# Performance work log

Hardware: AMD Instinct MI355X
Metric: run time of the kernel (lower is better)

Reference implementation:

```python
import jax, jax.numpy as jnp
import numpy as np

B, S, D, H, L, V = 8, 512, 1024, 16, 12, 30145
FF = 4 * D
NL = 2  # n_langs
EPS = 1e-12


def _ln(x, g, b):
    m = jnp.mean(x, axis=-1, keepdims=True)
    v = jnp.var(x, axis=-1, keepdims=True)
    return (x - m) * jax.lax.rsqrt(v + EPS) * g + b


def setup_inputs() -> dict:
    key = jax.random.key(0)
    ks = iter(jax.random.split(key, 32))
    std, estd = 0.02, 0.02
    d = {
        "input_ids": jax.random.randint(next(ks), (B, S), 0, V),
        "langs": jax.random.randint(next(ks), (B, S), 0, NL),
        "attention_mask": jnp.ones((B, S), jnp.float32),
        "word_emb": jax.random.normal(next(ks), (V, D), jnp.float32) * estd,
        "pos_emb": jax.random.normal(next(ks), (S, D), jnp.float32) * estd,
        "lang_emb": jax.random.normal(next(ks), (NL, D), jnp.float32) * estd,
        "ln_emb_g": jnp.ones((D,), jnp.float32),
        "ln_emb_b": jnp.zeros((D,), jnp.float32),
        "Wq": jax.random.normal(next(ks), (L, D, D), jnp.float32) * std,
        "bq": jnp.zeros((L, D), jnp.float32),
        "Wk": jax.random.normal(next(ks), (L, D, D), jnp.float32) * std,
        "bk": jnp.zeros((L, D), jnp.float32),
        "Wv": jax.random.normal(next(ks), (L, D, D), jnp.float32) * std,
        "bv": jnp.zeros((L, D), jnp.float32),
        "Wo": jax.random.normal(next(ks), (L, D, D), jnp.float32) * std,
        "bo": jnp.zeros((L, D), jnp.float32),
        "ln1_g": jnp.ones((L, D), jnp.float32),
        "ln1_b": jnp.zeros((L, D), jnp.float32),
        "W1": jax.random.normal(next(ks), (L, D, FF), jnp.float32) * std,
        "b1": jnp.zeros((L, FF), jnp.float32),
        "W2": jax.random.normal(next(ks), (L, FF, D), jnp.float32) * std,
        "b2": jnp.zeros((L, D), jnp.float32),
        "ln2_g": jnp.ones((L, D), jnp.float32),
        "ln2_b": jnp.zeros((L, D), jnp.float32),
    }
    return d


def reference(input_ids, langs, attention_mask, word_emb, pos_emb, lang_emb,
              ln_emb_g, ln_emb_b, Wq, bq, Wk, bk, Wv, bv, Wo, bo,
              ln1_g, ln1_b, W1, b1, W2, b2, ln2_g, ln2_b):
    dh = D // H
    scale = 1.0 / np.sqrt(dh).astype(np.float32)
    # embeddings: word + position + language, then LayerNorm, then pad-mask
    x = word_emb[input_ids] + pos_emb[None, :, :] + lang_emb[langs]  # [B,S,D]
    x = _ln(x, ln_emb_g, ln_emb_b)
    fmask = attention_mask  # [B,S], 1=keep
    x = x * fmask[:, :, None]
    neg = (-1e30) * (1.0 - fmask)[:, None, None, :]  # [B,1,1,S] additive mask

    def layer(x, p):
        Wq_, bq_, Wk_, bk_, Wv_, bv_, Wo_, bo_, g1, gb1, W1_, b1_, W2_, b2_, g2, gb2 = p
        q = ((x @ Wq_ + bq_) * scale).reshape(B, S, H, dh)
        k = (x @ Wk_ + bk_).reshape(B, S, H, dh)
        v = (x @ Wv_ + bv_).reshape(B, S, H, dh)
        scores = jnp.einsum('bqhd,bkhd->bhqk', q, k) + neg
        w = jax.nn.softmax(scores, axis=-1)
        ctx = jnp.einsum('bhqk,bkhd->bqhd', w, v).reshape(B, S, D)
        x = _ln(x + ctx @ Wo_ + bo_, g1, gb1)
        h = jax.nn.gelu(x @ W1_ + b1_, approximate=False)  # erf gelu as in source
        x = _ln(x + h @ W2_ + b2_, g2, gb2)
        x = x * fmask[:, :, None]
        return x, None

    params = (Wq, bq, Wk, bk, Wv, bv, Wo, bo, ln1_g, ln1_b, W1, b1, W2, b2, ln2_g, ln2_b)
    x, _ = jax.lax.scan(layer, x, params)
    return x
```

## Files before the change

### kernel.cpp

```cpp
#include <hip/hip_runtime.h>
#include <math.h>

typedef float  f32x4  __attribute__((ext_vector_type(4)));
typedef __bf16 bf16x8 __attribute__((ext_vector_type(8)));
typedef __bf16 bf16x4 __attribute__((ext_vector_type(4)));

#define DEV __device__ __forceinline__

DEV f32x4 mfma16(bf16x8 a, bf16x8 b, f32x4 c) {
    return __builtin_amdgcn_mfma_f32_16x16x32_bf16(a, b, c, 0, 0, 0);
}

DEV void async16(const void* g, void* l) {
    __builtin_amdgcn_global_load_lds((const __attribute__((address_space(1))) void*)g,
                                     (__attribute__((address_space(3))) void*)l, 16, 0, 0);
}

constexpr int B_  = 8;
constexpr int S_  = 512;
constexpr int D_  = 1024;
constexpr int H_  = 16;
constexpr int FF_ = 4096;
constexpr int ROWS = B_ * S_;

__global__ __launch_bounds__(256)
void embed_ln_kernel(const int* __restrict__ ids, const int* __restrict__ lgs,
                     const float* __restrict__ fmask,
                     const float* __restrict__ wemb, const float* __restrict__ pemb,
                     const float* __restrict__ lemb,
                     const float* __restrict__ g, const float* __restrict__ bb,
                     __bf16* __restrict__ xb)
{
    __shared__ float2 red[4];
    const int row = blockIdx.x;
    const int s   = row & (S_ - 1);
    const int t   = threadIdx.x;
    const int lane = t & 63, w = t >> 6;
    const int id = ids[row], lg = lgs[row];

    float4 wv = *(const float4*)(wemb + ((size_t)id << 10) + t * 4);
    float4 pv = *(const float4*)(pemb + ((size_t)s  << 10) + t * 4);
    float4 lv = *(const float4*)(lemb + ((size_t)lg << 10) + t * 4);
    float a[4] = { wv.x + pv.x + lv.x, wv.y + pv.y + lv.y,
                   wv.z + pv.z + lv.z, wv.w + pv.w + lv.w };

    float sm = a[0] + a[1] + a[2] + a[3];
    float sq = a[0]*a[0] + a[1]*a[1] + a[2]*a[2] + a[3]*a[3];
#pragma unroll
    for (int o = 32; o > 0; o >>= 1) { sm += __shfl_down(sm, o); sq += __shfl_down(sq, o); }
    if (lane == 0) red[w] = make_float2(sm, sq);
    __syncthreads();
    float ts = red[0].x + red[1].x + red[2].x + red[3].x;
    float tq = red[0].y + red[1].y + red[2].y + red[3].y;
    float mean = ts * (1.0f / D_);
    float var  = tq * (1.0f / D_) - mean * mean;
    float rs   = rsqrtf(var + 1e-12f);
    float fm   = fmask[row];

    float4 gv = *(const float4*)(g  + t * 4);
    float4 bv = *(const float4*)(bb + t * 4);
    bf16x4 ob;
    ob[0] = (__bf16)(((a[0]-mean)*rs*gv.x + bv.x) * fm);
    ob[1] = (__bf16)(((a[1]-mean)*rs*gv.y + bv.y) * fm);
    ob[2] = (__bf16)(((a[2]-mean)*rs*gv.z + bv.z) * fm);
    ob[3] = (__bf16)(((a[3]-mean)*rs*gv.w + bv.w) * fm);
    *(bf16x4*)(xb + ((size_t)row << 10) + t * 4) = ob;
}

template<int NP>
__global__ __launch_bounds__(128)
void ln_resN_kernel(const __bf16* __restrict__ xres, const __bf16* __restrict__ yp,
                    const float* __restrict__ g, const float* __restrict__ bb,
                    const float* __restrict__ fmask,
                    __bf16* __restrict__ xb_out, float* __restrict__ fout)
{
    constexpr size_t MN = (size_t)ROWS * D_;
    __shared__ float2 red[2];
    const int row = blockIdx.x;
    const int t   = threadIdx.x;
    const int lane = t & 63, w = t >> 6;
    const size_t base = ((size_t)row << 10) + t * 8;

    bf16x8 xv = *(const bf16x8*)(xres + base);
    float a[8];
#pragma unroll
    for (int j = 0; j < 8; ++j) a[j] = (float)xv[j];
#pragma unroll
    for (int pslice = 0; pslice < NP; ++pslice) {
        bf16x8 yv = *(const bf16x8*)(yp + base + (size_t)pslice * MN);
#pragma unroll
        for (int j = 0; j < 8; ++j) a[j] += (float)yv[j];
    }

    float sm = 0.f, sq = 0.f;
#pragma unroll
    for (int j = 0; j < 8; ++j) { sm += a[j]; sq += a[j] * a[j]; }
#pragma unroll
    for (int o = 32; o > 0; o >>= 1) { sm += __shfl_down(sm, o); sq += __shfl_down(sq, o); }
    if (lane == 0) red[w] = make_float2(sm, sq);
    __syncthreads();
    float ts = red[0].x + red[1].x;
    float tq = red[0].y + red[1].y;
    float mean = ts * (1.0f / D_);
    float var  = tq * (1.0f / D_) - mean * mean;
    float rs   = rsqrtf(var + 1e-12f);
    float fm   = fmask ? fmask[row] : 1.0f;

    float4 gv0 = *(const float4*)(g  + t * 8);
    float4 gv1 = *(const float4*)(g  + t * 8 + 4);
    float4 bv0 = *(const float4*)(bb + t * 8);
    float4 bv1 = *(const float4*)(bb + t * 8 + 4);
    float gg[8] = { gv0.x, gv0.y, gv0.z, gv0.w, gv1.x, gv1.y, gv1.z, gv1.w };
    float bbv[8] = { bv0.x, bv0.y, bv0.z, bv0.w, bv1.x, bv1.y, bv1.z, bv1.w };

    float o[8];
    bf16x8 ob;
#pragma unroll
    for (int j = 0; j < 8; ++j) {
        o[j] = ((a[j] - mean) * rs * gg[j] + bbv[j]) * fm;
        ob[j] = (__bf16)o[j];
    }
    *(bf16x8*)(xb_out + base) = ob;
    if (fout) {
        *(float4*)(fout + base)     = make_float4(o[0], o[1], o[2], o[3]);
        *(float4*)(fout + base + 4) = make_float4(o[4], o[5], o[6], o[7]);
    }
}

__global__ __launch_bounds__(256)
void conv_all_kernel(const float* __restrict__ Wq, const float* __restrict__ Wk,
                     const float* __restrict__ Wv, const float* __restrict__ Wo,
                     const float* __restrict__ W1, const float* __restrict__ W2,
                     __bf16* __restrict__ qkvT, __bf16* __restrict__ woT,
                     __bf16* __restrict__ w1T, __bf16* __restrict__ w2T)
{
    __shared__ unsigned int tile32[64 * 34];
    const int id = blockIdx.x;
    const int l  = id / 768;
    int t = id - l * 768;
    const size_t woff = (size_t)l * D_ * D_;
    const size_t foff = (size_t)l * D_ * FF_;
    const float* src; __bf16* dst; int K, N;
    if (t < 256) {
        const int m = t >> 6; t &= 63; K = 1024; N = 1024;
        src = ((m == 0) ? Wq : (m == 1) ? Wk : (m == 2) ? Wv : Wo) + woff;
        dst = (m == 3) ? (woT + woff)
                       : (qkvT + (size_t)l * 3 * D_ * D_ + (size_t)m * D_ * D_);
    } else if (t < 512) {
        t -= 256; K = 1024; N = 4096; src = W1 + foff; dst = w1T + foff;
    } else {
        t -= 512; K = 4096; N = 1024; src = W2 + foff; dst = w2T + foff;
    }
    const int ksup = K >> 8;
    const int tk = t % ksup, tn = t / ksup;
    const int k0s = tk << 8, n0t = tn << 6;
    const int tt = threadIdx.x;

    const int kp = tt >> 4;
    const int nq = tt & 15;
    const int swzw = (nq >> 2) << 2;
    const int nr = tt >> 3;
    const int kc = tt & 7;

    bf16x8 ob[2][4];
#pragma unroll
    for (int i4 = 0; i4 < 4; ++i4) {
        const int k0t = k0s + i4 * 64;
#pragma unroll
        for (int i = 0; i < 2; ++i) {
            const int k0 = i * 32 + kp * 2;
            const float4 r0 = *(const float4*)(src + (size_t)(k0t + k0)     * N + n0t + nq * 4);
            const float4 r1 = *(const float4*)(src + (size_t)(k0t + k0 + 1) * N + n0t + nq * 4);
            const int j = (i * 16 + kp) ^ swzw;
            const float lo[4] = { r0.x, r0.y, r0.z, r0.w };
            const float hi[4] = { r1.x, r1.y, r1.z, r1.w };
#pragma unroll
            for (int c = 0; c < 4; ++c) {
                const int n = nq * 4 + c;
                union { unsigned int u; __bf16 b[2]; } pk;
                pk.b[0] = (__bf16)lo[c];
                pk.b[1] = (__bf16)hi[c];
                tile32[n * 34 + j] = pk.u;
            }
        }
        __syncthreads();
#pragma unroll
        for (int pp = 0; pp < 2; ++pp) {
            const int n = pp * 32 + nr;
            const int jb = (kc * 4) ^ ((n >> 4) << 2);
            const unsigned int* tp = tile32 + n * 34 + jb;
            union { unsigned int u[4]; bf16x8 v; } o;
            o.u[0] = tp[0]; o.u[1] = tp[1]; o.u[2] = tp[2]; o.u[3] = tp[3];
            ob[pp][i4] = o.v;
        }
        __syncthreads();
    }
#pragma unroll
    for (int pp = 0; pp < 2; ++pp) {
        const int n = pp * 32 + nr;
        __bf16* drow = dst + (size_t)(n0t + n) * K + k0s + kc * 8;
#pragma unroll
        for (int i4 = 0; i4 < 4; ++i4)
            *(bf16x8*)(drow + i4 * 64) = ob[pp][i4];
    }
}

template<int EPI>
__global__ __launch_bounds__(512, 2)
void gemm256_kernel(const __bf16* __restrict__ A, const __bf16* __restrict__ Bt,
                    const float* __restrict__ b0, const float* __restrict__ b1,
                    const float* __restrict__ b2,
                    __bf16* __restrict__ o0, __bf16* __restrict__ o1,
                    __bf16* __restrict__ o2, __bf16* __restrict__ oP,
                    int M, int N, int K, int Kloc, int nTn, int tiles)
{
    __shared__ __bf16 lds[65536];
    const int tid  = threadIdx.x;
    const int lane = tid & 63;
    const int w    = tid >> 6;
    const int wr   = w >> 2, wc = w & 3;

    const int nwg = gridDim.x, bid = blockIdx.x;
    const int cpx = nwg >> 3;
    const int bswz = (bid & 7) * cpx + (bid >> 3);
    const int slice = bswz / tiles;
    const int tile  = bswz % tiles;
    const int bm = tile / nTn, bn = tile % nTn;
    const int m0 = bm << 8, n0 = bn << 8;
    const int ks = slice * Kloc;

    const int rrT = tid >> 3;
    const size_t swzK  = (size_t)(((tid & 7) ^ (rrT & 7)) * 8);
    const size_t aoff0 = (size_t)rrT * K + swzK;
    const size_t boff0 = (size_t)((rrT >> 5) * 64 + (rrT & 31)) * K + swzK;
    const size_t boff1 = (size_t)(((rrT >> 5) + 2) * 64 + (rrT & 31)) * K + swzK;
    const int wub = w * 512;

    const int aread = (wr * 64 + (lane & 15)) * 64;
    const int bread = (wc * 32 + (lane & 15)) * 64;
    const int csw0 = ((      (lane >> 4) * 16) ^ ((lane & 7) << 4)) >> 1;
    const int csw1 = ((64 +  (lane >> 4) * 16) ^ ((lane & 7) << 4)) >> 1;

    f32x4 acc[8][4] = {};
    bf16x8 a_[4][2], b_[2][2];

#define ST_A(p,h,kt) do {                                                     \
    const size_t gb = (size_t)(m0 + (h) * 64) * K + (kt);                     \
    async16(A + gb + aoff0,                  lds + ((p)*2+(h))*8192 + wub);   \
    async16(A + gb + (size_t)128*K + aoff0,  lds + ((p)*2+(h))*8192 + 4096 + wub); \
} while (0)
#define ST_B(p,h,kt) do {                                                     \
    const size_t gb = (size_t)(n0 + (h) * 32) * K + (kt);                     \
    async16(Bt + gb + boff0, lds + 32768 + ((p)*2+(h))*8192 + wub);           \
    async16(Bt + gb + boff1, lds + 32768 + ((p)*2+(h))*8192 + 4096 + wub);    \
} while (0)
#define DS_A(p,h) do {                                                        \
    const __bf16* base_ = lds + ((p)*2+(h))*8192 + aread;                     \
    _Pragma("unroll") for (int m_ = 0; m_ < 4; ++m_) {                        \
        a_[m_][0] = *(const bf16x8*)(base_ + m_*1024 + csw0);                 \
        a_[m_][1] = *(const bf16x8*)(base_ + m_*1024 + csw1);                 \
    }                                                                         \
} while (0)
#define DS_B(p,h) do {                                                        \
    const __bf16* base_ = lds + 32768 + ((p)*2+(h))*8192 + bread;             \
    _Pragma("unroll") for (int n_ = 0; n_ < 2; ++n_) {                        \
        b_[n_][0] = *(const bf16x8*)(base_ + n_*1024 + csw0);                 \
        b_[n_][1] = *(const bf16x8*)(base_ + n_*1024 + csw1);                 \
    }                                                                         \
} while (0)
#define MM(mb,nb) do {                                                        \
    _Pragma("unroll") for (int m_ = 0; m_ < 4; ++m_)                          \
    _Pragma("unroll") for (int n_ = 0; n_ < 2; ++n_)                          \
    _Pragma("unroll") for (int k_ = 0; k_ < 2; ++k_)                          \
        acc[(mb)+m_][(nb)+n_] = mfma16(a_[m_][k_], b_[n_][k_], acc[(mb)+m_][(nb)+n_]); \
} while (0)
#define SYNC do { __builtin_amdgcn_s_barrier();                               \
    asm volatile("s_waitcnt lgkmcnt(0)" ::: "memory");                        \
    __builtin_amdgcn_s_setprio(1); } while (0)
#define PEND do { __builtin_amdgcn_s_setprio(0);                              \
    __builtin_amdgcn_s_barrier(); } while (0)

    ST_A(0,0, ks);      ST_B(0,1, ks);      ST_A(0,1, ks);      ST_B(0,0, ks);
    ST_A(1,0, ks + 64); ST_B(1,1, ks + 64); ST_A(1,1, ks + 64);
    asm volatile("s_waitcnt vmcnt(6)" ::: "memory");
    __builtin_amdgcn_s_barrier();

    const int nIter = Kloc >> 7;
    for (int i = 0; i < nIter; ++i) {
        const bool nl = (i != nIter - 1);
        const int kt1 = ks + (2*i+1) * 64;
        const int kt2 = ks + (2*i+2) * 64;
        const int kt3 = kt2 + 64;
        DS_A(0,0); DS_B(0,0); ST_B(1,0,kt1);
        SYNC; MM(0,0); PEND;
        DS_B(0,1); if (nl) ST_A(0,0,kt2);
        SYNC; MM(0,2); PEND;
        DS_A(0,1); if (nl) ST_B(0,1,kt2);
        SYNC; MM(4,2); PEND;
        DS_B(0,0); if (nl) ST_A(0,1,kt2);
        SYNC; MM(4,0);
        __builtin_amdgcn_s_setprio(0);
        if (nl) asm volatile("s_waitcnt vmcnt(6)" ::: "memory");
        else    asm volatile("s_waitcnt vmcnt(0)" ::: "memory");
        __builtin_amdgcn_s_barrier();
        DS_A(1,0); DS_B(1,0); if (nl) ST_B(0,0,kt2);
        SYNC; MM(0,0); PEND;
        DS_B(1,1); if (nl) ST_A(1,0,kt3);
        SYNC; MM(0,2); PEND;
        DS_A(1,1); if (nl) ST_B(1,1,kt3);
        SYNC; MM(4,2); PEND;
        DS_B(1,0); if (nl) ST_A(1,1,kt3);
        SYNC; MM(4,0);
        __builtin_amdgcn_s_setprio(0);
        if (nl) asm volatile("s_waitcnt vmcnt(6)" ::: "memory");
        __builtin_amdgcn_s_barrier();
    }
#undef ST_A
#undef ST_B
#undef DS_A
#undef DS_B
#undef MM
#undef SYNC
#undef PEND

    const int mrow = m0 + wr * 128 + (lane >> 4) * 4;
    const int ncol = n0 + wc * 64 + (lane & 15);
    if (EPI == 0) {
        const int sel = n0 >> 10;
        const int nc = ncol & 1023;
        if (sel < 2) {
            __bf16* out = (sel == 0) ? o0 : o1;
            const float* bp = (sel == 0) ? b0 : b1;
            const float scl = (sel == 0) ? 0.125f : 1.0f;
#pragma unroll
            for (int ni = 0; ni < 4; ++ni) {
                const float bvv = bp[nc + ni * 16];
#pragma unroll
                for (int mi = 0; mi < 8; ++mi)
#pragma unroll
                    for (int r = 0; r < 4; ++r)
                        out[(size_t)(mrow + mi * 16 + r) * D_ + nc + ni * 16] =
                            (__bf16)((acc[mi][ni][r] + bvv) * scl);
            }
        } else {
#pragma unroll
            for (int ni = 0; ni < 4; ++ni) {
                const int dhf = nc + ni * 16;
                const float bvv = b2[dhf];
                const int hh = dhf >> 6, dh = dhf & 63;
#pragma unroll
                for (int mi = 0; mi < 8; ++mi) {
                    const int gm0 = mrow + mi * 16;
                    const int bb_ = gm0 >> 9, s0 = gm0 & 511;
                    bf16x4 pk;
#pragma unroll
                    for (int r = 0; r < 4; ++r) pk[r] = (__bf16)(acc[mi][ni][r] + bvv);
                    *(bf16x4*)(o2 + ((size_t)((bb_ * 16 + hh) * 64 + dh) << 9) + s0) = pk;
                }
            }
        }
    } else if (EPI == 2) {
#pragma unroll
        for (int ni = 0; ni < 4; ++ni) {
            const float bvv = b0[ncol + ni * 16];
#pragma unroll
            for (int mi = 0; mi < 8; ++mi)
#pragma unroll
                for (int r = 0; r < 4; ++r) {
                    float v = acc[mi][ni][r] + bvv;
                    float u2 = 1.5957691216f * v * (1.0f + 0.044715f * v * v);
                    float ge = v / (1.0f + __expf(-u2));
                    o0[(size_t)(mrow + mi * 16 + r) * N + ncol + ni * 16] = (__bf16)ge;
                }
        }
    } else {
        __bf16* Y = oP + (size_t)slice * M * N;
#pragma unroll
        for (int ni = 0; ni < 4; ++ni) {
            const float bvv = (slice == 0) ? b0[ncol + ni * 16] : 0.0f;
#pragma unroll
            for (int mi = 0; mi < 8; ++mi)
#pragma unroll
                for (int r = 0; r < 4; ++r)
                    Y[(size_t)(mrow + mi * 16 + r) * N + ncol + ni * 16] =
                        (__bf16)(acc[mi][ni][r] + bvv);
        }
    }
}

__global__ __launch_bounds__(512, 1)
void attn_kernel(const __bf16* __restrict__ q, const __bf16* __restrict__ k,
                 const __bf16* __restrict__ vT, const float* __restrict__ fmask,
                 __bf16* __restrict__ ctx)
{
    __shared__ __bf16 Ks[512 * 64];
    __shared__ __bf16 Vt[64 * 512];
    const int bid = blockIdx.x;
    const int qt = bid & 3, h = (bid >> 2) & 15, b = bid >> 6;
    const int tid = threadIdx.x, lane = tid & 63, w = tid >> 6;
    const int g = lane >> 4, q15 = lane & 15, r7 = lane & 7;

    const __bf16* kbase  = k  + ((size_t)b * S_) * D_ + h * 64;
    const __bf16* vTbase = vT + ((size_t)((b * 16 + h) * 64) << 9);
    const float*  fmb    = fmask + b * S_;
    char* kl = (char*)Ks + (tid & ~63) * 16;
    char* vl = (char*)Vt + (tid & ~63) * 16;
    const int srow  = tid >> 3;
    const int sslot = (tid & 7) ^ (srow & 7);

#pragma unroll
    for (int i = 0; i < 8; ++i) {
        const int s = i * 64 + srow;
        async16(kbase + (size_t)s * D_ + sslot * 8, kl + i * 8192);
    }
#pragma unroll
    for (int i = 0; i < 8; ++i) {
        const int d = i * 8 + w;
        async16(vTbase + ((size_t)d << 9) + (((tid & 63) ^ (d & 7)) << 3), vl + i * 8192);
    }

    const __bf16* qbase = q + ((size_t)b * S_ + qt * 128 + w * 16) * D_ + h * 64;
    const bf16x8 qf0 = *(const bf16x8*)(qbase + (size_t)q15 * D_ + g * 8);
    const bf16x8 qf1 = *(const bf16x8*)(qbase + (size_t)q15 * D_ + 32 + g * 8);

    f32x4 sc[32];
#pragma unroll
    for (int i = 0; i < 32; ++i) { sc[i][0] = 0.f; sc[i][1] = 0.f; sc[i][2] = 0.f; sc[i][3] = 0.f; }

    __syncthreads();
#pragma unroll
    for (int nf = 0; nf < 32; ++nf) {
        const __bf16* kr = Ks + (nf * 16 + q15) * 64;
        const bf16x8 kf0 = *(const bf16x8*)(kr + ((g ^ r7) << 3));
        const bf16x8 kf1 = *(const bf16x8*)(kr + (((g + 4) ^ r7) << 3));
        sc[nf] = mfma16(kf0, qf0, sc[nf]);
        sc[nf] = mfma16(kf1, qf1, sc[nf]);
    }

    float mx = -3e38f;
#pragma unroll
    for (int i = 0; i < 32; ++i) {
        const float4 fm4 = *(const float4*)(fmb + i * 16 + 4 * g);
        sc[i][0] += (fm4.x - 1.0f) * 1e30f;
        sc[i][1] += (fm4.y - 1.0f) * 1e30f;
        sc[i][2] += (fm4.z - 1.0f) * 1e30f;
        sc[i][3] += (fm4.w - 1.0f) * 1e30f;
        mx = fmaxf(mx, fmaxf(fmaxf(sc[i][0], sc[i][1]), fmaxf(sc[i][2], sc[i][3])));
    }
    mx = fmaxf(mx, __shfl_xor(mx, 16));
    mx = fmaxf(mx, __shfl_xor(mx, 32));
    float sum = 0.f;
#pragma unroll
    for (int i = 0; i < 32; ++i)
#pragma unroll
        for (int r = 0; r < 4; ++r) { float pp = __expf(sc[i][r] - mx); sc[i][r] = pp; sum += pp; }
    sum += __shfl_xor(sum, 16);
    sum += __shfl_xor(sum, 32);
    const float inv = 1.0f / sum;

    __bf16* P = Ks + w * 4096;
    f32x4 co[4] = {};
#define WR_P(c) do { _Pragma("unroll") for (int i_ = 0; i_ < 16; ++i_) {      \
        bf16x4 pk;                                                            \
        _Pragma("unroll") for (int r = 0; r < 4; ++r) pk[r] = (__bf16)sc[(c)*16+i_][r]; \
        *(bf16x4*)(P + q15 * 256 + ((i_ * 16 + 4 * g) ^ (8 * r7))) = pk; } } while (0)
#define PV(c) do { _Pragma("unroll") for (int kt = 0; kt < 8; ++kt) {         \
        const bf16x8 pf = *(const bf16x8*)(P + q15 * 256 + ((kt * 32 + 8 * g) ^ (8 * r7))); \
        _Pragma("unroll") for (int nf = 0; nf < 4; ++nf) {                    \
            const int d_ = nf * 16 + q15;                                     \
            const bf16x8 vf = *(const bf16x8*)(Vt + d_ * 512 +                \
                (((c) * 256 + kt * 32 + 8 * g) ^ (8 * r7)));                  \
            co[nf] = mfma16(vf, pf, co[nf]); } } } while (0)

    __syncthreads();
    WR_P(0);
    __syncthreads();
    PV(0);
    __syncthreads();
    WR_P(1);
    __syncthreads();
    PV(1);
#undef WR_P
#undef PV

    __bf16* cb = ctx + ((size_t)b * S_ + qt * 128 + w * 16 + q15) * D_ + h * 64;
#pragma unroll
    for (int nf = 0; nf < 4; ++nf) {
        bf16x4 o4;
#pragma unroll
        for (int r = 0; r < 4; ++r) o4[r] = (__bf16)(co[nf][r] * inv);
        *(bf16x4*)(cb + nf * 16 + 4 * g) = o4;
    }
}

extern "C" void kernel_launch(void* const* d_in, const int* in_sizes, int n_in,
                              void* d_out, int out_size, void* d_ws, size_t ws_size,
                              hipStream_t stream)
{
    (void)in_sizes; (void)n_in; (void)out_size; (void)ws_size;
    const int*   ids   = (const int*)d_in[0];
    const int*   lgs   = (const int*)d_in[1];
    const float* amask = (const float*)d_in[2];
    const float* wemb  = (const float*)d_in[3];
    const float* pemb  = (const float*)d_in[4];
    const float* lemb  = (const float*)d_in[5];
    const float* lng   = (const float*)d_in[6];
    const float* lnbv  = (const float*)d_in[7];
    const float* Wq = (const float*)d_in[8];  const float* bq = (const float*)d_in[9];
    const float* Wk = (const float*)d_in[10]; const float* bk = (const float*)d_in[11];
    const float* Wv = (const float*)d_in[12]; const float* bv = (const float*)d_in[13];
    const float* Wo = (const float*)d_in[14]; const float* bo = (const float*)d_in[15];
    const float* g1 = (const float*)d_in[16]; const float* be1 = (const float*)d_in[17];
    const float* W1 = (const float*)d_in[18]; const float* b1 = (const float*)d_in[19];
    const float* W2 = (const float*)d_in[20]; const float* b2 = (const float*)d_in[21];
    const float* g2 = (const float*)d_in[22]; const float* be2 = (const float*)d_in[23];

    char* p = (char*)d_ws;
    auto take = [&](size_t n) { char* r = p; p += (n + 255) & ~(size_t)255; return r; };
    __bf16* xb    = (__bf16*)take((size_t)ROWS * D_ * 2);
    __bf16* qb    = (__bf16*)take((size_t)ROWS * D_ * 2);
    __bf16* kb    = (__bf16*)take((size_t)ROWS * D_ * 2);
    __bf16* vT    = (__bf16*)take((size_t)ROWS * D_ * 2);
    __bf16* cxb   = (__bf16*)take((size_t)ROWS * D_ * 2);
    __bf16* hb    = (__bf16*)take((size_t)ROWS * FF_ * 2);
    __bf16* ybp   = (__bf16*)take((size_t)4 * ROWS * D_ * 2);
    __bf16* wqkvT = (__bf16*)take((size_t)12 * 3 * D_ * D_ * 2);
    __bf16* woT   = (__bf16*)take((size_t)12 * D_ * D_ * 2);
    __bf16* w1T   = (__bf16*)take((size_t)12 * D_ * FF_ * 2);
    __bf16* w2T   = (__bf16*)take((size_t)12 * FF_ * D_ * 2);

    const int gQKV = (ROWS / 256) * (3 * D_ / 256);
    const int gF1  = (ROWS / 256) * (FF_ / 256);
    const int gF2  = 4 * (ROWS / 256) * (D_ / 256);
    const int gWo  = 4 * (ROWS / 256) * (D_ / 256);

    conv_all_kernel<<<12 * 768, 256, 0, stream>>>(Wq, Wk, Wv, Wo, W1, W2,
                                                  wqkvT, woT, w1T, w2T);

    embed_ln_kernel<<<ROWS, 256, 0, stream>>>(ids, lgs, amask, wemb, pemb, lemb, lng, lnbv, xb);

    for (int l = 0; l < 12; ++l) {
        __bf16* wqkvL = wqkvT + (size_t)l * 3 * D_ * D_;
        __bf16* woL   = woT   + (size_t)l * D_ * D_;
        __bf16* w1L   = w1T   + (size_t)l * D_ * FF_;
        __bf16* w2L   = w2T   + (size_t)l * FF_ * D_;

        gemm256_kernel<0><<<gQKV, 512, 0, stream>>>(xb, wqkvL, bq + l * D_, bk + l * D_, bv + l * D_,
                                                    qb, kb, vT, nullptr,
                                                    ROWS, 3 * D_, D_, D_, 12, gQKV);

        attn_kernel<<<B_ * H_ * (S_ / 128), 512, 0, stream>>>(qb, kb, vT, amask, cxb);

        gemm256_kernel<3><<<gWo, 512, 0, stream>>>(cxb, woL, bo + l * D_, nullptr, nullptr,
                                                   nullptr, nullptr, nullptr, ybp,
                                                   ROWS, D_, D_, D_ / 4, 4, 64);
        ln_resN_kernel<4><<<ROWS, 128, 0, stream>>>(xb, ybp, g1 + l * D_, be1 + l * D_,
                                                    nullptr, xb, nullptr);

        gemm256_kernel<2><<<gF1, 512, 0, stream>>>(xb, w1L, b1 + l * FF_, nullptr, nullptr,
                                                   hb, nullptr, nullptr, nullptr,
                                                   ROWS, FF_, D_, D_, 16, gF1);
        gemm256_kernel<3><<<gF2, 512, 0, stream>>>(hb, w2L, b2 + l * D_, nullptr, nullptr,
                                                   nullptr, nullptr, nullptr, ybp,
                                                   ROWS, D_, FF_, D_, 4, 64);

        float* dst = (l == 11) ? (float*)d_out : nullptr;
        ln_resN_kernel<4><<<ROWS, 128, 0, stream>>>(xb, ybp, g2 + l * D_, be2 + l * D_,
                                                    amask, xb, dst);
    }
}
```

Before: 2.467 ms.

## Replace split-K Wo GEMM with 128x128 tile GEMM and widen weight-convert tiles

The attention-output projection previously used the 256x256 GEMM with 4-way split-K, writing four bf16 partial slabs that the following LayerNorm summed. It now uses a new 128x128-tile GEMM that runs over the full K (256 workgroups) and writes one slab, so the LayerNorm reads a single partial. This removes the partial-sum traffic, but each tile uses a simple single-buffered async-LDS loop with a sync on every K step. The weight conversion/transpose kernel also moves from 64-wide to 128-wide N tiles with one LDS pass per workgroup, halving the block count but using a much larger LDS tile.

```diff
diff --git a/kernel.cpp b/kernel.cpp
--- a/kernel.cpp
+++ b/kernel.cpp
@@ -134,74 +134,58 @@
                      __bf16* __restrict__ qkvT, __bf16* __restrict__ woT,
                      __bf16* __restrict__ w1T, __bf16* __restrict__ w2T)
 {
-    __shared__ unsigned int tile32[64 * 34];
+    __shared__ unsigned int tile32[128 * 130];
     const int id = blockIdx.x;
-    const int l  = id / 768;
-    int t = id - l * 768;
+    const int l  = id / 384;
+    int t = id - l * 384;
     const size_t woff = (size_t)l * D_ * D_;
     const size_t foff = (size_t)l * D_ * FF_;
     const float* src; __bf16* dst; int K, N;
-    if (t < 256) {
-        const int m = t >> 6; t &= 63; K = 1024; N = 1024;
+    if (t < 128) {
+        const int m = t >> 5; t &= 31; K = 1024; N = 1024;
         src = ((m == 0) ? Wq : (m == 1) ? Wk : (m == 2) ? Wv : Wo) + woff;
         dst = (m == 3) ? (woT + woff)
                        : (qkvT + (size_t)l * 3 * D_ * D_ + (size_t)m * D_ * D_);
-    } else if (t < 512) {
-        t -= 256; K = 1024; N = 4096; src = W1 + foff; dst = w1T + foff;
+    } else if (t < 256) {
+        t -= 128; K = 1024; N = 4096; src = W1 + foff; dst = w1T + foff;
     } else {
-        t -= 512; K = 4096; N = 1024; src = W2 + foff; dst = w2T + foff;
+        t -= 256; K = 4096; N = 1024; src = W2 + foff; dst = w2T + foff;
     }
     const int ksup = K >> 8;
     const int tk = t % ksup, tn = t / ksup;
-    const int k0s = tk << 8, n0t = tn << 6;
+    const int k0s = tk << 8, n0t = tn << 7;
     const int tt = threadIdx.x;
 
-    const int kp = tt >> 4;
-    const int nq = tt & 15;
-    const int swzw = (nq >> 2) << 2;
-    const int nr = tt >> 3;
-    const int kc = tt & 7;
-
-    bf16x8 ob[2][4];
-#pragma unroll
-    for (int i4 = 0; i4 < 4; ++i4) {
-        const int k0t = k0s + i4 * 64;
-#pragma unroll
-        for (int i = 0; i < 2; ++i) {
-            const int k0 = i * 32 + kp * 2;
-            const float4 r0 = *(const float4*)(src + (size_t)(k0t + k0)     * N + n0t + nq * 4);
-            const float4 r1 = *(const float4*)(src + (size_t)(k0t + k0 + 1) * N + n0t + nq * 4);
-            const int j = (i * 16 + kp) ^ swzw;
-            const float lo[4] = { r0.x, r0.y, r0.z, r0.w };
-            const float hi[4] = { r1.x, r1.y, r1.z, r1.w };
-#pragma unroll
-            for (int c = 0; c < 4; ++c) {
-                const int n = nq * 4 + c;
-                union { unsigned int u; __bf16 b[2]; } pk;
-                pk.b[0] = (__bf16)lo[c];
-                pk.b[1] = (__bf16)hi[c];
-                tile32[n * 34 + j] = pk.u;
-            }
+    const int lane32 = tt & 31;
+    const int pair   = tt >> 5;
+    const int swzr   = (lane32 >> 2) << 2;
+
+#pragma unroll
+    for (int it = 0; it < 16; ++it) {
+        const int rl = it * 16 + pair * 2;
+        const float4 f0 = *(const float4*)(src + (size_t)(k0s + rl)     * N + n0t + lane32 * 4);
+        const float4 f1 = *(const float4*)(src + (size_t)(k0s + rl + 1) * N + n0t + lane32 * 4);
+        const int j = (rl >> 1) ^ swzr;
+        const float lo[4] = { f0.x, f0.y, f0.z, f0.w };
+        const float hi[4] = { f1.x, f1.y, f1.z, f1.w };
+#pragma unroll
+        for (int c = 0; c < 4; ++c) {
+            union { unsigned int u; __bf16 b[2]; } pk;
+            pk.b[0] = (__bf16)lo[c];
+            pk.b[1] = (__bf16)hi[c];
+            tile32[(lane32 * 4 + c) * 130 + j] = pk.u;
         }
-        __syncthreads();
-#pragma unroll
-        for (int pp = 0; pp < 2; ++pp) {
-            const int n = pp * 32 + nr;
-            const int jb = (kc * 4) ^ ((n >> 4) << 2);
-            const unsigned int* tp = tile32 + n * 34 + jb;
-            union { unsigned int u[4]; bf16x8 v; } o;
-            o.u[0] = tp[0]; o.u[1] = tp[1]; o.u[2] = tp[2]; o.u[3] = tp[3];
-            ob[pp][i4] = o.v;
-        }
-        __syncthreads();
-    }
-#pragma unroll
-    for (int pp = 0; pp < 2; ++pp) {
-        const int n = pp * 32 + nr;
-        __bf16* drow = dst + (size_t)(n0t + n) * K + k0s + kc * 8;
-#pragma unroll
-        for (int i4 = 0; i4 < 4; ++i4)
-            *(bf16x8*)(drow + i4 * 64) = ob[pp][i4];
+    }
+    __syncthreads();
+
+#pragma unroll
+    for (int it = 0; it < 16; ++it) {
+        const int n = it * 8 + pair;
+        const int jb = (lane32 * 4) ^ ((n >> 4) << 2);
+        const unsigned int* tp = tile32 + n * 130 + jb;
+        union { unsigned int u[4]; bf16x8 v; } o;
+        o.u[0] = tp[0]; o.u[1] = tp[1]; o.u[2] = tp[2]; o.u[3] = tp[3];
+        *(bf16x8*)(dst + (size_t)(n0t + n) * K + k0s + lane32 * 8) = o.v;
     }
 }
 
@@ -388,6 +372,72 @@
     }
 }
 
+__global__ __launch_bounds__(256, 2)
+void gemm_kernel(const __bf16* __restrict__ A, const __bf16* __restrict__ Bt,
+                 const float* __restrict__ bias, __bf16* __restrict__ Cb,
+                 int M, int N, int K)
+{
+    __shared__ __bf16 As[128 * 64];
+    __shared__ __bf16 Bs[128 * 64];
+    const int tid = threadIdx.x;
+    const int lane = tid & 63;
+    const int w = tid >> 6, wr = w >> 1, wc = w & 1;
+    const int nT = N >> 7;
+    const int nwg = gridDim.x;
+    const int bid = blockIdx.x;
+    const int cpx = nwg >> 3;
+    const int bswz = (bid & 7) * cpx + (bid >> 3);
+    const int bm = bswz / nT, bn = bswz % nT;
+    const int m0 = bm << 7, n0 = bn << 7;
+
+    f32x4 acc[4][4] = {};
+
+    const int chr = tid >> 3, chc = tid & 7;
+    const __bf16* ga = A  + (size_t)(m0 + chr) * K + chc * 8;
+    const __bf16* gb = Bt + (size_t)(n0 + chr) * K + chc * 8;
+    char* la = (char*)As + (tid & ~63) * 16;
+    char* lb = (char*)Bs + (tid & ~63) * 16;
+
+    const __bf16* arow = As + (wr * 64 + (lane & 15)) * 64 + (lane >> 4) * 8;
+    const __bf16* brow = Bs + (wc * 64 + (lane & 15)) * 64 + (lane >> 4) * 8;
+
+    for (int k0 = 0; k0 < K; k0 += 64) {
+#pragma unroll
+        for (int i = 0; i < 4; ++i) {
+            async16(ga + (size_t)(i * 32) * K + k0, la + i * 4096);
+            async16(gb + (size_t)(i * 32) * K + k0, lb + i * 4096);
+        }
+        __syncthreads();
+#pragma unroll
+        for (int kk = 0; kk < 2; ++kk) {
+            bf16x8 af[4], bf[4];
+#pragma unroll
+            for (int i = 0; i < 4; ++i) af[i] = *(const bf16x8*)(arow + i * 16 * 64 + kk * 32);
+#pragma unroll
+            for (int i = 0; i < 4; ++i) bf[i] = *(const bf16x8*)(brow + i * 16 * 64 + kk * 32);
+#pragma unroll
+            for (int mi = 0; mi < 4; ++mi)
+#pragma unroll
+                for (int ni = 0; ni < 4; ++ni)
+                    acc[mi][ni] = mfma16(af[mi], bf[ni], acc[mi][ni]);
+        }
+        __syncthreads();
+    }
+
+    const int mb = m0 + wr * 64 + ((lane >> 4) * 4);
+    const int nb = n0 + wc * 64 + (lane & 15);
+#pragma unroll
+    for (int ni = 0; ni < 4; ++ni) {
+        const float bvv = bias[nb + ni * 16];
+#pragma unroll
+        for (int mi = 0; mi < 4; ++mi)
+#pragma unroll
+            for (int r = 0; r < 4; ++r)
+                Cb[(size_t)(mb + mi * 16 + r) * N + nb + ni * 16] =
+                    (__bf16)(acc[mi][ni][r] + bvv);
+    }
+}
+
 __global__ __launch_bounds__(512, 1)
 void attn_kernel(const __bf16* __restrict__ q, const __bf16* __restrict__ k,
                  const __bf16* __restrict__ vT, const float* __restrict__ fmask,
@@ -532,9 +582,9 @@
     const int gQKV = (ROWS / 256) * (3 * D_ / 256);
     const int gF1  = (ROWS / 256) * (FF_ / 256);
     const int gF2  = 4 * (ROWS / 256) * (D_ / 256);
-    const int gWo  = 4 * (ROWS / 256) * (D_ / 256);
-
-    conv_all_kernel<<<12 * 768, 256, 0, stream>>>(Wq, Wk, Wv, Wo, W1, W2,
+    const int gWo  = (ROWS / 128) * (D_ / 128);
+
+    conv_all_kernel<<<12 * 384, 256, 0, stream>>>(Wq, Wk, Wv, Wo, W1, W2,
                                                   wqkvT, woT, w1T, w2T);
 
     embed_ln_kernel<<<ROWS, 256, 0, stream>>>(ids, lgs, amask, wemb, pemb, lemb, lng, lnbv, xb);
@@ -551,10 +601,8 @@
 
         attn_kernel<<<B_ * H_ * (S_ / 128), 512, 0, stream>>>(qb, kb, vT, amask, cxb);
 
-        gemm256_kernel<3><<<gWo, 512, 0, stream>>>(cxb, woL, bo + l * D_, nullptr, nullptr,
-                                                   nullptr, nullptr, nullptr, ybp,
-                                                   ROWS, D_, D_, D_ / 4, 4, 64);
-        ln_resN_kernel<4><<<ROWS, 128, 0, stream>>>(xb, ybp, g1 + l * D_, be1 + l * D_,
+        gemm_kernel<<<gWo, 256, 0, stream>>>(cxb, woL, bo + l * D_, ybp, ROWS, D_, D_);
+        ln_resN_kernel<1><<<ROWS, 128, 0, stream>>>(xb, ybp, g1 + l * D_, be1 + l * D_,
                                                     nullptr, xb, nullptr);
 
         gemm256_kernel<2><<<gF1, 512, 0, stream>>>(xb, w1L, b1 + l * FF_, nullptr, nullptr,
```

Measured after the change: 2.468 ms, median of 2. Within noise of the previous version (+0.1%).
